# Kernel tuning notes

Hardware: AMD Instinct MI355X
Metric: run time of the kernel (lower is better)

The kernel has to match this reference:

```python
import jax, jax.numpy as jnp
import numpy as np

B, T, C = 4, 1024, 768
H, HS = 12, 64           # num_heads, head_size
VD = 2 * HS              # value dim per head


def setup_inputs() -> dict:
    key = jax.random.key(0)
    ks = jax.random.split(key, 16)
    s = 0.02
    inp = {
        "x": jax.random.normal(ks[0], (B, T, C), jnp.float32),
        "Wq1": jax.random.normal(ks[1], (H, C, HS), jnp.float32) * s,
        "Wk1": jax.random.normal(ks[2], (H, C, HS), jnp.float32) * s,
        "Wq2": jax.random.normal(ks[3], (H, C, HS), jnp.float32) * s,
        "Wk2": jax.random.normal(ks[4], (H, C, HS), jnp.float32) * s,
        "Wv": jax.random.normal(ks[5], (H, C, VD), jnp.float32) * s,
        "lq1": jax.random.normal(ks[6], (H, HS), jnp.float32) * 0.1,
        "lk1": jax.random.normal(ks[7], (H, HS), jnp.float32) * 0.1,
        "lq2": jax.random.normal(ks[8], (H, HS), jnp.float32) * 0.1,
        "lk2": jax.random.normal(ks[9], (H, HS), jnp.float32) * 0.1,
        "gn_w": jnp.ones((H * VD,), jnp.float32),
        "gn_b": jnp.zeros((H * VD,), jnp.float32),
        "Wp": jax.random.normal(ks[10], (C, H * VD), jnp.float32) * s,
        "bp": jnp.zeros((C,), jnp.float32),
        "layer_idx": 3,
    }
    return inp


def _diff_attn(x, Wq1, Wk1, Wq2, Wk2, Wv, lq1, lk1, lq2, lk2,
               gn_w, gn_b, Wp, bp, layer_idx):
    Bc, Tc, _ = x.shape
    scale = 1.0 / jnp.sqrt(jnp.float32(HS))
    # per-head projections: [B,H,T,HS]
    q1 = jnp.einsum('btc,hcd->bhtd', x, Wq1)
    k1 = jnp.einsum('btc,hcd->bhtd', x, Wk1)
    q2 = jnp.einsum('btc,hcd->bhtd', x, Wq2)
    k2 = jnp.einsum('btc,hcd->bhtd', x, Wk2)
    v = jnp.einsum('btc,hce->bhte', x, Wv)           # [B,H,T,2HS]
    mask = jnp.tril(jnp.ones((Tc, Tc), bool))         # causal
    neg = jnp.float32(-jnp.inf)
    a1 = jnp.einsum('bhtd,bhsd->bhts', q1, k1) * scale
    a2 = jnp.einsum('bhtd,bhsd->bhts', q2, k2) * scale
    a1 = jax.nn.softmax(jnp.where(mask, a1, neg), axis=-1)
    a2 = jax.nn.softmax(jnp.where(mask, a2, neg), axis=-1)
    # dynamic lambda init, per get_lambda
    li = jnp.float32(layer_idx)
    dyn = 0.8 - 0.6 * jnp.exp(-0.3 * (li - 1.0))
    lam = jnp.mean(jnp.exp(lq1 * lk1) - jnp.exp(lq2 * lk2) + dyn, axis=-1)  # [H]
    diff = a1 - lam[None, :, None, None] * a2
    out = jnp.einsum('bhts,bhse->bhte', diff, v)      # [B,H,T,2HS]
    out = out.transpose(0, 2, 1, 3).reshape(Bc, Tc, H * VD)
    # GroupLayerNorm == full layernorm over last dim (unbiased=False var)
    mu = out.mean(-1, keepdims=True)
    var = jnp.mean((out - mu) ** 2, axis=-1, keepdims=True)
    out = (out - mu) / jnp.sqrt(var + 1e-5) * gn_w + gn_b
    out = out * 0.2  # (1 - lambda_init_buffer=0.8), buffer never updated
    return out @ Wp.T + bp


def reference(x, Wq1, Wk1, Wq2, Wk2, Wv, lq1, lk1, lq2, lk2,
              gn_w, gn_b, Wp, bp, layer_idx):
    return _diff_attn(x, Wq1, Wk1, Wq2, Wk2, Wv, lq1, lk1, lq2, lk2,
                      gn_w, gn_b, Wp, bp, layer_idx)
```

## Files before the change

### kernel.cpp

```cpp
#include <hip/hip_runtime.h>
#include <hip/hip_bf16.h>

#define Bc   4
#define Tc   1024
#define Cc   768
#define Hc   12
#define HSc  64
#define VDc  128
#define NQKV 4608
#define YLD  3072
#define NROWS 4096
#define HVD  1536

#define Q1OFF 0
#define K1OFF 768
#define Q2OFF 1536
#define K2OFF 2304

typedef __bf16 bf16x8 __attribute__((ext_vector_type(8)));
typedef float f32x4 __attribute__((ext_vector_type(4)));
typedef unsigned int u32x4 __attribute__((ext_vector_type(4)));

#define EXP2SCALE 0.18033688011112042f

static __device__ __forceinline__ float bf2f(unsigned short s) {
    return __uint_as_float(((unsigned int)s) << 16);
}
static __device__ __forceinline__ unsigned short f2bf(float f) {
    unsigned int u = __float_as_uint(f);
    unsigned int r = (u + 0x7FFFu + ((u >> 16) & 1u)) >> 16;
    return (unsigned short)r;
}
static __device__ __forceinline__ unsigned int pack2bf(float lo, float hi) {
    unsigned int a = (__float_as_uint(lo) + 0x8000u) >> 16;
    unsigned int b = (__float_as_uint(hi) + 0x8000u) & 0xFFFF0000u;
    return a | b;
}
static __device__ __forceinline__ float fast_exp2(float x) {
    float r;
    asm("v_exp_f32 %0, %1" : "=v"(r) : "v"(x));
    return r;
}

static __device__ __forceinline__ void load16_lds(const void* g, void* l) {
    __builtin_amdgcn_global_load_lds(
        (const __attribute__((address_space(1))) void*)g,
        (__attribute__((address_space(3))) void*)l, 16, 0, 0);
}

__global__ __launch_bounds__(256) void prep(
    const float* __restrict__ x, const float* __restrict__ Wp,
    const float* __restrict__ lq1, const float* __restrict__ lk1,
    const float* __restrict__ lq2, const float* __restrict__ lk2,
    const int* __restrict__ layer_idx,
    const float* __restrict__ Wq1, const float* __restrict__ Wk1,
    const float* __restrict__ Wq2, const float* __restrict__ Wk2,
    const float* __restrict__ Wv,
    unsigned short* __restrict__ Xb, unsigned short* __restrict__ Wpb,
    float* __restrict__ lam, float* __restrict__ outz,
    unsigned short* __restrict__ WcatT)
{
    __shared__ float tile[64][65];
    int bid = blockIdx.x, tid = threadIdx.x;
    if (bid < 3072) {
        size_t i = (size_t)bid * 256 + tid;
        float4 v = *(const float4*)(x + i * 4);
        ushort4 u;
        u.x = f2bf(v.x); u.y = f2bf(v.y); u.z = f2bf(v.z); u.w = f2bf(v.w);
        *(ushort4*)(Xb + i * 4) = u;
    } else if (bid < 4224) {
        size_t i = (size_t)(bid - 3072) * 256 + tid;
        float4 v = *(const float4*)(Wp + i * 4);
        ushort4 u;
        u.x = f2bf(v.x); u.y = f2bf(v.y); u.z = f2bf(v.z); u.w = f2bf(v.w);
        *(ushort4*)(Wpb + i * 4) = u;
    } else if (bid < 4236) {
        if (tid < 64) {
            int h = bid - 4224, l = tid;
            float li = (float)layer_idx[0];
            float dyn = 0.8f - 0.6f * expf(-0.3f * (li - 1.0f));
            int i = h * HSc + l;
            float v = expf(lq1[i] * lk1[i]) - expf(lq2[i] * lk2[i]) + dyn;
            #pragma unroll
            for (int off = 32; off; off >>= 1) v += __shfl_xor(v, off);
            if (l == 0) lam[h] = v * (1.0f / 64.0f);
        }
    } else if (bid < 7308) {
        size_t i = (size_t)(bid - 4236) * 256 + tid;
        float4 z = {0.f, 0.f, 0.f, 0.f};
        *(float4*)(outz + i * 4) = z;
    } else {
        int t = bid - 7308;
        int kt = t % 12, nt = t / 12;
        int k0 = kt * 64, n0 = nt * 64;
        const float* src;
        int stride;
        if (n0 < 3072) {
            int which = n0 / 768, m = n0 - which * 768, h = m >> 6;
            const float* W = (which == 0) ? Wq1 : (which == 1) ? Wk1 : (which == 2) ? Wq2 : Wk2;
            src = W + ((size_t)h * 768 + k0) * 64;
            stride = 64;
        } else {
            int rel = n0 - 3072, h = rel >> 7, e0 = rel & 127;
            src = Wv + ((size_t)h * 768 + k0) * 128 + e0;
            stride = 128;
        }
        for (int i = tid; i < 4096; i += 256) {
            int kl = i >> 6, dl = i & 63;
            tile[dl][kl] = src[(size_t)kl * stride + dl];
        }
        __syncthreads();
        for (int i = tid; i < 4096; i += 256) {
            int nl = i >> 6, kl = i & 63;
            WcatT[(size_t)(n0 + nl) * 768 + k0 + kl] = f2bf(tile[nl][kl]);
        }
    }
}

template<int TN, int KD, int LDC, bool OUT_BIAS, bool SPLITV, int KSPLIT>
__global__ __launch_bounds__(256) void gemm_mfma(
    const unsigned short* __restrict__ A, const unsigned short* __restrict__ Bt,
    unsigned short* __restrict__ Cb, float* __restrict__ Cf,
    const float* __restrict__ bias, unsigned short* __restrict__ VtOut)
{
    constexpr int BN = TN * 32;
    constexpr int JB = TN / 2;
    constexpr int ASLOT = 128 * 64;
    constexpr int SLOT  = ASLOT + BN * 64;
    __shared__ unsigned short ring[2 * SLOT];
    int tid = threadIdx.x, lane = tid & 63, w = tid >> 6;
    int wm = w >> 1, wn = w & 1;

    int bid = blockIdx.x;
    int xcd = bid & 7;
    int idx = bid >> 3;
    int ks = 0;
    if (KSPLIT == 2) { ks = idx & 1; idx >>= 1; }
    int mi  = idx & 3;
    int ni  = idx >> 2;
    int m0 = (xcd * 4 + mi) * 128;
    int n0 = ni * BN;
    constexpr int KLOC = KD / KSPLIT;
    const int kBase = ks * KLOC;

    int lr = lane >> 2, lq = lane & 3;
    const unsigned short* gA[2];
    const unsigned short* gB[JB];
    #pragma unroll
    for (int j = 0; j < 2; ++j) {
        int row = w * 32 + j * 16 + lr;
        int qg = lq ^ ((row >> 1) & 3);
        gA[j] = A + (size_t)(m0 + row) * KD + kBase + qg * 8;
    }
    #pragma unroll
    for (int j = 0; j < JB; ++j) {
        int row = w * (JB * 16) + j * 16 + lr;
        int qg = lq ^ ((row >> 1) & 3);
        gB[j] = Bt + (size_t)(n0 + row) * KD + kBase + qg * 8;
    }

    int rr = lane & 15, qd = lane >> 4;
    int aOff[4], bOff[TN];
    #pragma unroll
    for (int i = 0; i < 4; ++i) {
        int row = wm * 64 + i * 16 + rr;
        int qs = qd ^ ((row >> 1) & 3);
        aOff[i] = row * 32 + qs * 8;
    }
    #pragma unroll
    for (int t = 0; t < TN; ++t) {
        int row = wn * (TN * 16) + t * 16 + rr;
        int qs = qd ^ ((row >> 1) & 3);
        bOff[t] = row * 32 + qs * 8;
    }

    auto stageG = [&](int k, int slot) {
        unsigned short* s = ring + slot * SLOT;
        int k64 = k * 64;
        load16_lds(gA[0] + k64,      s + (w * 2 + 0) * 512);
        load16_lds(gA[1] + k64,      s + (w * 2 + 1) * 512);
        load16_lds(gA[0] + k64 + 32, s + 4096 + (w * 2 + 0) * 512);
        load16_lds(gA[1] + k64 + 32, s + 4096 + (w * 2 + 1) * 512);
        #pragma unroll
        for (int j = 0; j < JB; ++j) {
            load16_lds(gB[j] + k64,      s + ASLOT + (w * JB + j) * 512);
            load16_lds(gB[j] + k64 + 32, s + ASLOT + BN * 32 + (w * JB + j) * 512);
        }
    };

    f32x4 acc[4][TN];
    #pragma unroll
    for (int i = 0; i < 4; ++i)
        #pragma unroll
        for (int t = 0; t < TN; ++t) acc[i][t] = {0.f, 0.f, 0.f, 0.f};

    constexpr int NT = KLOC / 64;
    stageG(0, 0);
    for (int k = 0; k < NT; ++k) {
        asm volatile("s_waitcnt vmcnt(0)\n\ts_barrier" ::: "memory");
        const unsigned short* s = ring + (k & 1) * SLOT;
        if (k + 1 < NT) stageG(k + 1, (k + 1) & 1);

        bf16x8 af0[4], af1[4], bf0[TN], bf1[TN];
        #pragma unroll
        for (int i = 0; i < 4; ++i) {
            af0[i] = *(const bf16x8*)(s + aOff[i]);
            af1[i] = *(const bf16x8*)(s + 4096 + aOff[i]);
        }
        #pragma unroll
        for (int t = 0; t < TN; ++t) {
            bf0[t] = *(const bf16x8*)(s + ASLOT + bOff[t]);
            bf1[t] = *(const bf16x8*)(s + ASLOT + BN * 32 + bOff[t]);
        }
        #pragma unroll
        for (int i = 0; i < 4; ++i)
            #pragma unroll
            for (int t = 0; t < TN; ++t) {
                acc[i][t] = __builtin_amdgcn_mfma_f32_16x16x32_bf16(af0[i], bf0[t], acc[i][t], 0, 0, 0);
                acc[i][t] = __builtin_amdgcn_mfma_f32_16x16x32_bf16(af1[i], bf1[t], acc[i][t], 0, 0, 0);
            }
    }

    #pragma unroll
    for (int t = 0; t < TN; ++t) {
        int col = n0 + wn * (TN * 16) + t * 16 + rr;
        if (SPLITV && col >= 3072) {
            int rel = col - 3072, hh = rel >> 7, e = rel & 127;
            #pragma unroll
            for (int i = 0; i < 4; ++i) {
                int row0 = m0 + wm * 64 + i * 16 + qd * 4;
                int b = row0 >> 10, tt = row0 & 1023;
                ushort4 pk;
                pk.x = f2bf(acc[i][t][0]); pk.y = f2bf(acc[i][t][1]);
                pk.z = f2bf(acc[i][t][2]); pk.w = f2bf(acc[i][t][3]);
                *(ushort4*)&VtOut[(size_t)((b * Hc + hh) * 128 + e) * 1024 + tt] = pk;
            }
        } else if (KSPLIT == 2) {
            float bv = (OUT_BIAS && ks == 0) ? bias[col] : 0.f;
            #pragma unroll
            for (int i = 0; i < 4; ++i) {
                #pragma unroll
                for (int r = 0; r < 4; ++r) {
                    int row = m0 + wm * 64 + i * 16 + qd * 4 + r;
                    atomicAdd(&Cf[(size_t)row * LDC + col], acc[i][t][r] + bv);
                }
            }
        } else {
            float bv = OUT_BIAS ? bias[col] : 0.f;
            #pragma unroll
            for (int i = 0; i < 4; ++i) {
                #pragma unroll
                for (int r = 0; r < 4; ++r) {
                    int row = m0 + wm * 64 + i * 16 + qd * 4 + r;
                    if (OUT_BIAS)
                        Cf[(size_t)row * LDC + col] = acc[i][t][r] + bv;
                    else
                        Cb[(size_t)row * LDC + col] = f2bf(acc[i][t][r]);
                }
            }
        }
    }
}

__global__ __launch_bounds__(256) void diff_attn_mfma(
    const unsigned short* __restrict__ Y, const unsigned short* __restrict__ Vt,
    const float* __restrict__ lam_buf, unsigned short* __restrict__ attn)
{
    __shared__ __align__(16) unsigned short KVring[2 * 16384];

    int bh = blockIdx.x;
    int b = bh / Hc, h = bh - b * Hc;
    int g = 15 - (int)blockIdx.y;
    int tid = threadIdx.x, lane = tid & 63, wv = tid >> 6;
    int cl = lane & 15, qd = lane >> 4;
    float lamv = lam_buf[h];
    size_t rowbase = (size_t)(b * Tc) * YLD;
    const int hq = h * HSc;
    const unsigned short* VtB = Vt + ((size_t)bh << 17);
    const f32x4 zero4 = {0.f, 0.f, 0.f, 0.f};

    int sub = wv & 1;
    int off8[8];
    int dstoff;
    if (wv < 2) {
        int ksrow = lane >> 3;
        int ksch  = (lane & 7) ^ ksrow;
        #pragma unroll
        for (int j = 0; j < 8; ++j) {
            int moff = (j < 4) ? K1OFF : K2OFF;
            off8[j] = ((j & 3) * 8 + ksrow) * YLD + moff + hq + ksch * 8;
        }
        dstoff = 0;
    } else {
        int vsel = lane >> 2;
        int vsch = (lane & 3) ^ ((vsel >> 1) & 3);
        #pragma unroll
        for (int s = 0; s < 8; ++s)
            off8[s] = (s * 16 + vsel) * 1024 + vsch * 8;
        dstoff = 8192;
    }

    auto stage = [&](int i, int slot) {
        int kt = 2 * i + sub;
        char* base = (char*)KVring + slot * 32768 + sub * 16384 + dstoff;
        const unsigned short* g0 = (wv < 2)
            ? (Y + rowbase + (size_t)(kt * 32) * YLD)
            : (VtB + kt * 32);
        #pragma unroll
        for (int j = 0; j < 8; ++j)
            load16_lds(g0 + off8[j], base + j * 1024);
    };

    int kfo[2][4], vfo[8];
    #pragma unroll
    for (int c = 0; c < 2; ++c) {
        int row = c * 16 + cl;
        #pragma unroll
        for (int j = 0; j < 4; ++j)
            kfo[c][j] = (j >> 1) * 4096 + row * 128 +
                        ((((j & 1) * 4 + qd) ^ (row & 7)) << 4);
    }
    #pragma unroll
    for (int ec = 0; ec < 8; ++ec) {
        int e = ec * 16 + cl;
        vfo[ec] = 8192 + e * 64 + ((qd ^ ((e >> 1) & 3)) << 4);
    }

    int idxA = ((32 * (qd & 1)) + cl) * 4;
    int idxB = idxA + 64;
    bool loHalf = (qd < 2);

    int qrow = g * 64 + wv * 16;

    stage(0, 0);

    size_t qoff = rowbase + (size_t)(qrow + cl) * YLD;
    bf16x8 q1a = *(const bf16x8*)(Y + qoff + Q1OFF + hq + qd * 8);
    bf16x8 q1b = *(const bf16x8*)(Y + qoff + Q1OFF + hq + 32 + qd * 8);
    bf16x8 q2a = *(const bf16x8*)(Y + qoff + Q2OFF + hq + qd * 8);
    bf16x8 q2b = *(const bf16x8*)(Y + qoff + Q2OFF + hq + 32 + qd * 8);

    f32x4 O1[8], O2[8];
    #pragma unroll
    for (int ec = 0; ec < 8; ++ec) { O1[ec] = zero4; O2[ec] = zero4; }
    float l1s = 0.f, l2s = 0.f;

    auto transform = [&](f32x4 S1[2], f32x4 S2[2], int kt,
                         bf16x8& pa1o, bf16x8& pa2o) {
        if (kt * 32 + 31 > qrow) {
            #pragma unroll
            for (int c = 0; c < 2; ++c) {
                int lim = qrow + cl - kt * 32 - c * 16 - qd * 4;
                #pragma unroll
                for (int r = 0; r < 4; ++r) {
                    if (r > lim) { S1[c][r] = -1e30f; S2[c][r] = -1e30f; }
                }
            }
        }
        float p1v[2][4], p2v[2][4];
        #pragma unroll
        for (int c = 0; c < 2; ++c) {
            #pragma unroll
            for (int r = 0; r < 4; ++r) {
                p1v[c][r] = fast_exp2(S1[c][r] * EXP2SCALE);
                p2v[c][r] = fast_exp2(S2[c][r] * EXP2SCALE);
                l1s += p1v[c][r];
                l2s += p2v[c][r];
            }
        }
        unsigned int s1m[2][2], s2m[2][2];
        #pragma unroll
        for (int c = 0; c < 2; ++c) {
            s1m[c][0] = pack2bf(p1v[c][0], p1v[c][1]);
            s1m[c][1] = pack2bf(p1v[c][2], p1v[c][3]);
            s2m[c][0] = pack2bf(p2v[c][0], p2v[c][1]);
            s2m[c][1] = pack2bf(p2v[c][2], p2v[c][3]);
        }
        u32x4 U1, U2;
        {
            int a00 = __builtin_amdgcn_ds_bpermute(idxA, (int)s1m[0][0]);
            int a10 = __builtin_amdgcn_ds_bpermute(idxA, (int)s1m[1][0]);
            int a01 = __builtin_amdgcn_ds_bpermute(idxA, (int)s1m[0][1]);
            int a11 = __builtin_amdgcn_ds_bpermute(idxA, (int)s1m[1][1]);
            int b00 = __builtin_amdgcn_ds_bpermute(idxB, (int)s1m[0][0]);
            int b10 = __builtin_amdgcn_ds_bpermute(idxB, (int)s1m[1][0]);
            int b01 = __builtin_amdgcn_ds_bpermute(idxB, (int)s1m[0][1]);
            int b11 = __builtin_amdgcn_ds_bpermute(idxB, (int)s1m[1][1]);
            U1[0] = (unsigned)(loHalf ? a00 : a10);
            U1[1] = (unsigned)(loHalf ? a01 : a11);
            U1[2] = (unsigned)(loHalf ? b00 : b10);
            U1[3] = (unsigned)(loHalf ? b01 : b11);
        }
        {
            int a00 = __builtin_amdgcn_ds_bpermute(idxA, (int)s2m[0][0]);
            int a10 = __builtin_amdgcn_ds_bpermute(idxA, (int)s2m[1][0]);
            int a01 = __builtin_amdgcn_ds_bpermute(idxA, (int)s2m[0][1]);
            int a11 = __builtin_amdgcn_ds_bpermute(idxA, (int)s2m[1][1]);
            int b00 = __builtin_amdgcn_ds_bpermute(idxB, (int)s2m[0][0]);
            int b10 = __builtin_amdgcn_ds_bpermute(idxB, (int)s2m[1][0]);
            int b01 = __builtin_amdgcn_ds_bpermute(idxB, (int)s2m[0][1]);
            int b11 = __builtin_amdgcn_ds_bpermute(idxB, (int)s2m[1][1]);
            U2[0] = (unsigned)(loHalf ? a00 : a10);
            U2[1] = (unsigned)(loHalf ? a01 : a11);
            U2[2] = (unsigned)(loHalf ? b00 : b10);
            U2[3] = (unsigned)(loHalf ? b01 : b11);
        }
        pa1o = __builtin_bit_cast(bf16x8, U1);
        pa2o = __builtin_bit_cast(bf16x8, U2);
    };

    int NI = g + 1;
    for (int i = 0; i < NI; ++i) {
        asm volatile("s_waitcnt vmcnt(0)\n\ts_barrier" ::: "memory");
        const char* kbA = (const char*)KVring + (i & 1) * 32768;
        const char* kbB = kbA + 16384;
        if (i + 1 < NI) stage(i + 1, (i + 1) & 1);

        bf16x8 kfA[2][4], kfB[2][4];
        #pragma unroll
        for (int c = 0; c < 2; ++c)
            #pragma unroll
            for (int j = 0; j < 4; ++j) {
                kfA[c][j] = *(const bf16x8*)(kbA + kfo[c][j]);
                kfB[c][j] = *(const bf16x8*)(kbB + kfo[c][j]);
            }
        bf16x8 vfA[8];
        #pragma unroll
        for (int ec = 0; ec < 8; ++ec)
            vfA[ec] = *(const bf16x8*)(kbA + vfo[ec]);

        f32x4 S1A[2], S2A[2], S1B[2], S2B[2];
        #pragma unroll
        for (int c = 0; c < 2; ++c) {
            S1A[c] = zero4; S2A[c] = zero4; S1B[c] = zero4; S2B[c] = zero4;
        }
        #pragma unroll
        for (int c = 0; c < 2; ++c) {
            S1A[c] = __builtin_amdgcn_mfma_f32_16x16x32_bf16(kfA[c][0], q1a, S1A[c], 0, 0, 0);
            S1A[c] = __builtin_amdgcn_mfma_f32_16x16x32_bf16(kfA[c][1], q1b, S1A[c], 0, 0, 0);
            S2A[c] = __builtin_amdgcn_mfma_f32_16x16x32_bf16(kfA[c][2], q2a, S2A[c], 0, 0, 0);
            S2A[c] = __builtin_amdgcn_mfma_f32_16x16x32_bf16(kfA[c][3], q2b, S2A[c], 0, 0, 0);
            S1B[c] = __builtin_amdgcn_mfma_f32_16x16x32_bf16(kfB[c][0], q1a, S1B[c], 0, 0, 0);
            S1B[c] = __builtin_amdgcn_mfma_f32_16x16x32_bf16(kfB[c][1], q1b, S1B[c], 0, 0, 0);
            S2B[c] = __builtin_amdgcn_mfma_f32_16x16x32_bf16(kfB[c][2], q2a, S2B[c], 0, 0, 0);
            S2B[c] = __builtin_amdgcn_mfma_f32_16x16x32_bf16(kfB[c][3], q2b, S2B[c], 0, 0, 0);
        }

        bf16x8 pa1A, pa2A, pa1B, pa2B;
        transform(S1A, S2A, 2 * i, pa1A, pa2A);
        bf16x8 vfB[8];
        #pragma unroll
        for (int ec = 0; ec < 8; ++ec)
            vfB[ec] = *(const bf16x8*)(kbB + vfo[ec]);
        transform(S1B, S2B, 2 * i + 1, pa1B, pa2B);

        #pragma unroll
        for (int ec = 0; ec < 8; ++ec) {
            O1[ec] = __builtin_amdgcn_mfma_f32_16x16x32_bf16(pa1A, vfA[ec], O1[ec], 0, 0, 0);
            O2[ec] = __builtin_amdgcn_mfma_f32_16x16x32_bf16(pa2A, vfA[ec], O2[ec], 0, 0, 0);
        }
        #pragma unroll
        for (int ec = 0; ec < 8; ++ec) {
            O1[ec] = __builtin_amdgcn_mfma_f32_16x16x32_bf16(pa1B, vfB[ec], O1[ec], 0, 0, 0);
            O2[ec] = __builtin_amdgcn_mfma_f32_16x16x32_bf16(pa2B, vfB[ec], O2[ec], 0, 0, 0);
        }
    }

    l1s += __shfl_xor(l1s, 16); l1s += __shfl_xor(l1s, 32);
    l2s += __shfl_xor(l2s, 16); l2s += __shfl_xor(l2s, 32);
    float w1[4], w2[4];
    #pragma unroll
    for (int r = 0; r < 4; ++r) {
        float d1 = __shfl(l1s, qd * 4 + r);
        float d2 = __shfl(l2s, qd * 4 + r);
        w1[r] = 1.0f / d1;
        w2[r] = lamv / d2;
    }
    #pragma unroll
    for (int ec = 0; ec < 8; ++ec) {
        #pragma unroll
        for (int r = 0; r < 4; ++r) {
            size_t row = (size_t)(b * Tc + qrow + qd * 4 + r);
            attn[row * HVD + h * VDc + ec * 16 + cl] =
                f2bf(O1[ec][r] * w1[r] - O2[ec][r] * w2[r]);
        }
    }
}

__global__ __launch_bounds__(128) void ln_inplace(
    unsigned short* __restrict__ attn,
    const float* __restrict__ gnw, const float* __restrict__ gnb)
{
    int row = blockIdx.x, tid = threadIdx.x;
    unsigned short* p = attn + (size_t)row * HVD;
    float v[12];
    float s = 0.f, sq = 0.f;
    #pragma unroll
    for (int j = 0; j < 3; ++j) {
        int g = tid + j * 128;
        ushort4 u = *(const ushort4*)(p + g * 4);
        float x0 = bf2f(u.x), x1 = bf2f(u.y), x2 = bf2f(u.z), x3 = bf2f(u.w);
        v[j * 4 + 0] = x0; v[j * 4 + 1] = x1; v[j * 4 + 2] = x2; v[j * 4 + 3] = x3;
        s += x0 + x1 + x2 + x3;
        sq = fmaf(x0, x0, sq); sq = fmaf(x1, x1, sq);
        sq = fmaf(x2, x2, sq); sq = fmaf(x3, x3, sq);
    }
    #pragma unroll
    for (int off = 32; off; off >>= 1) { s += __shfl_xor(s, off); sq += __shfl_xor(sq, off); }
    __shared__ float ss[2], sqs[2];
    if ((tid & 63) == 0) { ss[tid >> 6] = s; sqs[tid >> 6] = sq; }
    __syncthreads();
    float S = ss[0] + ss[1], Q = sqs[0] + sqs[1];
    float mu = S * (1.0f / HVD);
    float rstd = rsqrtf(Q * (1.0f / HVD) - mu * mu + 1e-5f);
    #pragma unroll
    for (int j = 0; j < 3; ++j) {
        int g = tid + j * 128;
        float4 gw = *(const float4*)(gnw + g * 4);
        float4 gb = *(const float4*)(gnb + g * 4);
        ushort4 o;
        o.x = f2bf(((v[j * 4 + 0] - mu) * rstd * gw.x + gb.x) * 0.2f);
        o.y = f2bf(((v[j * 4 + 1] - mu) * rstd * gw.y + gb.y) * 0.2f);
        o.z = f2bf(((v[j * 4 + 2] - mu) * rstd * gw.z + gb.z) * 0.2f);
        o.w = f2bf(((v[j * 4 + 3] - mu) * rstd * gw.w + gb.w) * 0.2f);
        *(ushort4*)(p + g * 4) = o;
    }
}

extern "C" void kernel_launch(void* const* d_in, const int* in_sizes, int n_in,
                              void* d_out, int out_size, void* d_ws, size_t ws_size,
                              hipStream_t stream)
{
    const float* x   = (const float*)d_in[0];
    const float* Wq1 = (const float*)d_in[1];
    const float* Wk1 = (const float*)d_in[2];
    const float* Wq2 = (const float*)d_in[3];
    const float* Wk2 = (const float*)d_in[4];
    const float* Wv  = (const float*)d_in[5];
    const float* lq1 = (const float*)d_in[6];
    const float* lk1 = (const float*)d_in[7];
    const float* lq2 = (const float*)d_in[8];
    const float* lk2 = (const float*)d_in[9];
    const float* gnw = (const float*)d_in[10];
    const float* gnb = (const float*)d_in[11];
    const float* Wp  = (const float*)d_in[12];
    const float* bp  = (const float*)d_in[13];
    const int*   lidx = (const int*)d_in[14];
    float* out = (float*)d_out;

    char* w = (char*)d_ws;
    unsigned short* WcatT = (unsigned short*)(w);
    unsigned short* Xb    = (unsigned short*)(w + 7077888);
    unsigned short* Y     = (unsigned short*)(w + 13369344);
    unsigned short* VtW   = (unsigned short*)(w + 38535168);
    unsigned short* attn  = (unsigned short*)(w + 51118080);
    unsigned short* Wpb   = (unsigned short*)(w + 63700992);
    float* lam            = (float*)(w + 66060288);

    prep<<<dim3(8172), 256, 0, stream>>>(x, Wp, lq1, lk1, lq2, lk2, lidx,
                                         Wq1, Wk1, Wq2, Wk2, Wv,
                                         Xb, Wpb, lam, out, WcatT);
    gemm_mfma<4, 768, YLD, false, true, 1><<<dim3(1152), 256, 0, stream>>>(
        Xb, WcatT, Y, nullptr, nullptr, VtW);
    diff_attn_mfma<<<dim3(Bc * Hc, 16), 256, 0, stream>>>(Y, VtW, lam, attn);
    ln_inplace<<<dim3(NROWS), 128, 0, stream>>>(attn, gnw, gnb);
    gemm_mfma<2, HVD, Cc, true, false, 2><<<dim3(768), 256, 0, stream>>>(
        attn, Wpb, nullptr, out, bp, nullptr);
}
```

Measured before the change: 235.6 us.

## Load V fragments directly from global memory instead of staging through LDS

Only the K1/K2 tiles are staged into the shared-memory ring now, with all four waves splitting the K staging. Each wave reads its V fragments straight from global memory into registers at the start of every iteration. This halves LDS usage, which may allow more resident blocks, and removes the LDS round trip for V. In exchange each wave fetches V redundantly through the cache hierarchy. Global-load latency may also become exposed before the PV MFMAs, since those loads are issued in the same iteration they are consumed.

```diff
diff --git a/kernel.cpp b/kernel.cpp
--- a/kernel.cpp
+++ b/kernel.cpp
@@ -266,7 +266,7 @@
     const unsigned short* __restrict__ Y, const unsigned short* __restrict__ Vt,
     const float* __restrict__ lam_buf, unsigned short* __restrict__ attn)
 {
-    __shared__ __align__(16) unsigned short KVring[2 * 16384];
+    __shared__ __align__(16) unsigned short Kring[2 * 8192];
 
     int bh = blockIdx.x;
     int b = bh / Hc, h = bh - b * Hc;
@@ -279,39 +279,28 @@
     const unsigned short* VtB = Vt + ((size_t)bh << 17);
     const f32x4 zero4 = {0.f, 0.f, 0.f, 0.f};
 
-    int sub = wv & 1;
-    int off8[8];
-    int dstoff;
-    if (wv < 2) {
-        int ksrow = lane >> 3;
-        int ksch  = (lane & 7) ^ ksrow;
-        #pragma unroll
-        for (int j = 0; j < 8; ++j) {
-            int moff = (j < 4) ? K1OFF : K2OFF;
-            off8[j] = ((j & 3) * 8 + ksrow) * YLD + moff + hq + ksch * 8;
-        }
-        dstoff = 0;
-    } else {
-        int vsel = lane >> 2;
-        int vsch = (lane & 3) ^ ((vsel >> 1) & 3);
-        #pragma unroll
-        for (int s = 0; s < 8; ++s)
-            off8[s] = (s * 16 + vsel) * 1024 + vsch * 8;
-        dstoff = 8192;
+    int sub   = wv & 1;
+    int halfK = wv >> 1;
+    int ksrow = lane >> 3;
+    int ksch  = (lane & 7) ^ ksrow;
+    int offk[4];
+    #pragma unroll
+    for (int j = 0; j < 4; ++j) {
+        int seg = halfK * 4 + j;
+        int moff = (seg < 4) ? K1OFF : K2OFF;
+        offk[j] = ((seg & 3) * 8 + ksrow) * YLD + moff + hq + ksch * 8;
     }
 
     auto stage = [&](int i, int slot) {
         int kt = 2 * i + sub;
-        char* base = (char*)KVring + slot * 32768 + sub * 16384 + dstoff;
-        const unsigned short* g0 = (wv < 2)
-            ? (Y + rowbase + (size_t)(kt * 32) * YLD)
-            : (VtB + kt * 32);
-        #pragma unroll
-        for (int j = 0; j < 8; ++j)
-            load16_lds(g0 + off8[j], base + j * 1024);
+        char* base = (char*)Kring + slot * 16384 + sub * 8192 + halfK * 4096;
+        const unsigned short* g0 = Y + rowbase + (size_t)(kt * 32) * YLD;
+        #pragma unroll
+        for (int j = 0; j < 4; ++j)
+            load16_lds(g0 + offk[j], base + j * 1024);
     };
 
-    int kfo[2][4], vfo[8];
+    int kfo[2][4];
     #pragma unroll
     for (int c = 0; c < 2; ++c) {
         int row = c * 16 + cl;
@@ -320,11 +309,10 @@
             kfo[c][j] = (j >> 1) * 4096 + row * 128 +
                         ((((j & 1) * 4 + qd) ^ (row & 7)) << 4);
     }
-    #pragma unroll
-    for (int ec = 0; ec < 8; ++ec) {
-        int e = ec * 16 + cl;
-        vfo[ec] = 8192 + e * 64 + ((qd ^ ((e >> 1) & 3)) << 4);
-    }
+    int vgo[8];
+    #pragma unroll
+    for (int ec = 0; ec < 8; ++ec)
+        vgo[ec] = ((ec * 16 + cl) << 10) + qd * 8;
 
     int idxA = ((32 * (qd & 1)) + cl) * 4;
     int idxB = idxA + 64;
@@ -412,8 +400,16 @@
     int NI = g + 1;
     for (int i = 0; i < NI; ++i) {
         asm volatile("s_waitcnt vmcnt(0)\n\ts_barrier" ::: "memory");
-        const char* kbA = (const char*)KVring + (i & 1) * 32768;
-        const char* kbB = kbA + 16384;
+        const char* kbA = (const char*)Kring + (i & 1) * 16384;
+        const char* kbB = kbA + 8192;
+
+        bf16x8 vfA[8], vfB[8];
+        #pragma unroll
+        for (int ec = 0; ec < 8; ++ec)
+            vfA[ec] = *(const bf16x8*)(VtB + vgo[ec] + (2 * i) * 32);
+        #pragma unroll
+        for (int ec = 0; ec < 8; ++ec)
+            vfB[ec] = *(const bf16x8*)(VtB + vgo[ec] + (2 * i + 1) * 32);
         if (i + 1 < NI) stage(i + 1, (i + 1) & 1);
 
         bf16x8 kfA[2][4], kfB[2][4];
@@ -424,10 +420,6 @@
                 kfA[c][j] = *(const bf16x8*)(kbA + kfo[c][j]);
                 kfB[c][j] = *(const bf16x8*)(kbB + kfo[c][j]);
             }
-        bf16x8 vfA[8];
-        #pragma unroll
-        for (int ec = 0; ec < 8; ++ec)
-            vfA[ec] = *(const bf16x8*)(kbA + vfo[ec]);
 
         f32x4 S1A[2], S2A[2], S1B[2], S2B[2];
         #pragma unroll
@@ -448,10 +440,6 @@
 
         bf16x8 pa1A, pa2A, pa1B, pa2B;
         transform(S1A, S2A, 2 * i, pa1A, pa2A);
-        bf16x8 vfB[8];
-        #pragma unroll
-        for (int ec = 0; ec < 8; ++ec)
-            vfB[ec] = *(const bf16x8*)(kbB + vfo[ec]);
         transform(S1B, S2B, 2 * i + 1, pa1B, pa2B);
 
         #pragma unroll
```

Result: slower. 279.7 us (+18.7%).

## Double query rows per wave in diff attention to reuse K/V tiles

Applied to the files above, without the earlier changes.

Each workgroup now covers 128 query rows instead of 64, and each wave handles two 16-row query groups that share the K/V fragments loaded from LDS. This halves the number of workgroups and the K/V traffic per query row, since every staged tile serves twice as many rows. The cost is many more accumulator registers per wave, which lowers occupancy, plus fewer blocks (384) to spread across the CUs. Waves whose rows end before the current tile skip the compute but still join the barriers, so causal load imbalance inside a block grows.

```diff
diff --git a/kernel.cpp b/kernel.cpp
--- a/kernel.cpp
+++ b/kernel.cpp
@@ -270,7 +270,7 @@
 
     int bh = blockIdx.x;
     int b = bh / Hc, h = bh - b * Hc;
-    int g = 15 - (int)blockIdx.y;
+    int g = 7 - (int)blockIdx.y;
     int tid = threadIdx.x, lane = tid & 63, wv = tid >> 6;
     int cl = lane & 15, qd = lane >> 4;
     float lamv = lam_buf[h];
@@ -330,27 +330,36 @@
     int idxB = idxA + 64;
     bool loHalf = (qd < 2);
 
-    int qrow = g * 64 + wv * 16;
+    int qr0 = g * 128 + wv * 32;
+    int qr1 = qr0 + 16;
 
     stage(0, 0);
 
-    size_t qoff = rowbase + (size_t)(qrow + cl) * YLD;
-    bf16x8 q1a = *(const bf16x8*)(Y + qoff + Q1OFF + hq + qd * 8);
-    bf16x8 q1b = *(const bf16x8*)(Y + qoff + Q1OFF + hq + 32 + qd * 8);
-    bf16x8 q2a = *(const bf16x8*)(Y + qoff + Q2OFF + hq + qd * 8);
-    bf16x8 q2b = *(const bf16x8*)(Y + qoff + Q2OFF + hq + 32 + qd * 8);
-
-    f32x4 O1[8], O2[8];
-    #pragma unroll
-    for (int ec = 0; ec < 8; ++ec) { O1[ec] = zero4; O2[ec] = zero4; }
-    float l1s = 0.f, l2s = 0.f;
-
-    auto transform = [&](f32x4 S1[2], f32x4 S2[2], int kt,
-                         bf16x8& pa1o, bf16x8& pa2o) {
-        if (kt * 32 + 31 > qrow) {
+    size_t qoff0 = rowbase + (size_t)(qr0 + cl) * YLD;
+    bf16x8 q1a0 = *(const bf16x8*)(Y + qoff0 + Q1OFF + hq + qd * 8);
+    bf16x8 q1b0 = *(const bf16x8*)(Y + qoff0 + Q1OFF + hq + 32 + qd * 8);
+    bf16x8 q2a0 = *(const bf16x8*)(Y + qoff0 + Q2OFF + hq + qd * 8);
+    bf16x8 q2b0 = *(const bf16x8*)(Y + qoff0 + Q2OFF + hq + 32 + qd * 8);
+    size_t qoff1 = rowbase + (size_t)(qr1 + cl) * YLD;
+    bf16x8 q1a1 = *(const bf16x8*)(Y + qoff1 + Q1OFF + hq + qd * 8);
+    bf16x8 q1b1 = *(const bf16x8*)(Y + qoff1 + Q1OFF + hq + 32 + qd * 8);
+    bf16x8 q2a1 = *(const bf16x8*)(Y + qoff1 + Q2OFF + hq + qd * 8);
+    bf16x8 q2b1 = *(const bf16x8*)(Y + qoff1 + Q2OFF + hq + 32 + qd * 8);
+
+    f32x4 O1g0[8], O2g0[8], O1g1[8], O2g1[8];
+    #pragma unroll
+    for (int ec = 0; ec < 8; ++ec) {
+        O1g0[ec] = zero4; O2g0[ec] = zero4;
+        O1g1[ec] = zero4; O2g1[ec] = zero4;
+    }
+    float l1s0 = 0.f, l2s0 = 0.f, l1s1 = 0.f, l2s1 = 0.f;
+
+    auto transform = [&](f32x4 S1[2], f32x4 S2[2], int kt, int qrowX,
+                         float& l1s, float& l2s, bf16x8& pa1o, bf16x8& pa2o) {
+        if (kt * 32 + 31 > qrowX) {
             #pragma unroll
             for (int c = 0; c < 2; ++c) {
-                int lim = qrow + cl - kt * 32 - c * 16 - qd * 4;
+                int lim = qrowX + cl - kt * 32 - c * 16 - qd * 4;
                 #pragma unroll
                 for (int r = 0; r < 4; ++r) {
                     if (r > lim) { S1[c][r] = -1e30f; S2[c][r] = -1e30f; }
@@ -409,80 +418,112 @@
         pa2o = __builtin_bit_cast(bf16x8, U2);
     };
 
-    int NI = g + 1;
+    int NI = 2 * g + 2;
     for (int i = 0; i < NI; ++i) {
         asm volatile("s_waitcnt vmcnt(0)\n\ts_barrier" ::: "memory");
         const char* kbA = (const char*)KVring + (i & 1) * 32768;
         const char* kbB = kbA + 16384;
         if (i + 1 < NI) stage(i + 1, (i + 1) & 1);
 
-        bf16x8 kfA[2][4], kfB[2][4];
-        #pragma unroll
-        for (int c = 0; c < 2; ++c)
-            #pragma unroll
-            for (int j = 0; j < 4; ++j) {
-                kfA[c][j] = *(const bf16x8*)(kbA + kfo[c][j]);
-                kfB[c][j] = *(const bf16x8*)(kbB + kfo[c][j]);
-            }
-        bf16x8 vfA[8];
-        #pragma unroll
-        for (int ec = 0; ec < 8; ++ec)
-            vfA[ec] = *(const bf16x8*)(kbA + vfo[ec]);
-
-        f32x4 S1A[2], S2A[2], S1B[2], S2B[2];
-        #pragma unroll
-        for (int c = 0; c < 2; ++c) {
-            S1A[c] = zero4; S2A[c] = zero4; S1B[c] = zero4; S2B[c] = zero4;
-        }
-        #pragma unroll
-        for (int c = 0; c < 2; ++c) {
-            S1A[c] = __builtin_amdgcn_mfma_f32_16x16x32_bf16(kfA[c][0], q1a, S1A[c], 0, 0, 0);
-            S1A[c] = __builtin_amdgcn_mfma_f32_16x16x32_bf16(kfA[c][1], q1b, S1A[c], 0, 0, 0);
-            S2A[c] = __builtin_amdgcn_mfma_f32_16x16x32_bf16(kfA[c][2], q2a, S2A[c], 0, 0, 0);
-            S2A[c] = __builtin_amdgcn_mfma_f32_16x16x32_bf16(kfA[c][3], q2b, S2A[c], 0, 0, 0);
-            S1B[c] = __builtin_amdgcn_mfma_f32_16x16x32_bf16(kfB[c][0], q1a, S1B[c], 0, 0, 0);
-            S1B[c] = __builtin_amdgcn_mfma_f32_16x16x32_bf16(kfB[c][1], q1b, S1B[c], 0, 0, 0);
-            S2B[c] = __builtin_amdgcn_mfma_f32_16x16x32_bf16(kfB[c][2], q2a, S2B[c], 0, 0, 0);
-            S2B[c] = __builtin_amdgcn_mfma_f32_16x16x32_bf16(kfB[c][3], q2b, S2B[c], 0, 0, 0);
-        }
-
-        bf16x8 pa1A, pa2A, pa1B, pa2B;
-        transform(S1A, S2A, 2 * i, pa1A, pa2A);
-        bf16x8 vfB[8];
-        #pragma unroll
-        for (int ec = 0; ec < 8; ++ec)
-            vfB[ec] = *(const bf16x8*)(kbB + vfo[ec]);
-        transform(S1B, S2B, 2 * i + 1, pa1B, pa2B);
-
-        #pragma unroll
-        for (int ec = 0; ec < 8; ++ec) {
-            O1[ec] = __builtin_amdgcn_mfma_f32_16x16x32_bf16(pa1A, vfA[ec], O1[ec], 0, 0, 0);
-            O2[ec] = __builtin_amdgcn_mfma_f32_16x16x32_bf16(pa2A, vfA[ec], O2[ec], 0, 0, 0);
-        }
-        #pragma unroll
-        for (int ec = 0; ec < 8; ++ec) {
-            O1[ec] = __builtin_amdgcn_mfma_f32_16x16x32_bf16(pa1B, vfB[ec], O1[ec], 0, 0, 0);
-            O2[ec] = __builtin_amdgcn_mfma_f32_16x16x32_bf16(pa2B, vfB[ec], O2[ec], 0, 0, 0);
-        }
-    }
-
-    l1s += __shfl_xor(l1s, 16); l1s += __shfl_xor(l1s, 32);
-    l2s += __shfl_xor(l2s, 16); l2s += __shfl_xor(l2s, 32);
-    float w1[4], w2[4];
+        if (i * 64 <= qr1 + 15) {
+            bf16x8 kfA[2][4], kfB[2][4];
+            #pragma unroll
+            for (int c = 0; c < 2; ++c)
+                #pragma unroll
+                for (int j = 0; j < 4; ++j) {
+                    kfA[c][j] = *(const bf16x8*)(kbA + kfo[c][j]);
+                    kfB[c][j] = *(const bf16x8*)(kbB + kfo[c][j]);
+                }
+            bf16x8 vfA[8];
+            #pragma unroll
+            for (int ec = 0; ec < 8; ++ec)
+                vfA[ec] = *(const bf16x8*)(kbA + vfo[ec]);
+
+            f32x4 S1A0[2], S2A0[2], S1B0[2], S2B0[2];
+            f32x4 S1A1[2], S2A1[2], S1B1[2], S2B1[2];
+            #pragma unroll
+            for (int c = 0; c < 2; ++c) {
+                S1A0[c] = zero4; S2A0[c] = zero4; S1B0[c] = zero4; S2B0[c] = zero4;
+                S1A1[c] = zero4; S2A1[c] = zero4; S1B1[c] = zero4; S2B1[c] = zero4;
+            }
+            #pragma unroll
+            for (int c = 0; c < 2; ++c) {
+                S1A0[c] = __builtin_amdgcn_mfma_f32_16x16x32_bf16(kfA[c][0], q1a0, S1A0[c], 0, 0, 0);
+                S1A0[c] = __builtin_amdgcn_mfma_f32_16x16x32_bf16(kfA[c][1], q1b0, S1A0[c], 0, 0, 0);
+                S2A0[c] = __builtin_amdgcn_mfma_f32_16x16x32_bf16(kfA[c][2], q2a0, S2A0[c], 0, 0, 0);
+                S2A0[c] = __builtin_amdgcn_mfma_f32_16x16x32_bf16(kfA[c][3], q2b0, S2A0[c], 0, 0, 0);
+                S1A1[c] = __builtin_amdgcn_mfma_f32_16x16x32_bf16(kfA[c][0], q1a1, S1A1[c], 0, 0, 0);
+                S1A1[c] = __builtin_amdgcn_mfma_f32_16x16x32_bf16(kfA[c][1], q1b1, S1A1[c], 0, 0, 0);
+                S2A1[c] = __builtin_amdgcn_mfma_f32_16x16x32_bf16(kfA[c][2], q2a1, S2A1[c], 0, 0, 0);
+                S2A1[c] = __builtin_amdgcn_mfma_f32_16x16x32_bf16(kfA[c][3], q2b1, S2A1[c], 0, 0, 0);
+                S1B0[c] = __builtin_amdgcn_mfma_f32_16x16x32_bf16(kfB[c][0], q1a0, S1B0[c], 0, 0, 0);
+                S1B0[c] = __builtin_amdgcn_mfma_f32_16x16x32_bf16(kfB[c][1], q1b0, S1B0[c], 0, 0, 0);
+                S2B0[c] = __builtin_amdgcn_mfma_f32_16x16x32_bf16(kfB[c][2], q2a0, S2B0[c], 0, 0, 0);
+                S2B0[c] = __builtin_amdgcn_mfma_f32_16x16x32_bf16(kfB[c][3], q2b0, S2B0[c], 0, 0, 0);
+                S1B1[c] = __builtin_amdgcn_mfma_f32_16x16x32_bf16(kfB[c][0], q1a1, S1B1[c], 0, 0, 0);
+                S1B1[c] = __builtin_amdgcn_mfma_f32_16x16x32_bf16(kfB[c][1], q1b1, S1B1[c], 0, 0, 0);
+                S2B1[c] = __builtin_amdgcn_mfma_f32_16x16x32_bf16(kfB[c][2], q2a1, S2B1[c], 0, 0, 0);
+                S2B1[c] = __builtin_amdgcn_mfma_f32_16x16x32_bf16(kfB[c][3], q2b1, S2B1[c], 0, 0, 0);
+            }
+
+            bf16x8 pa1A0, pa2A0, pa1A1, pa2A1, pa1B0, pa2B0, pa1B1, pa2B1;
+            transform(S1A0, S2A0, 2 * i, qr0, l1s0, l2s0, pa1A0, pa2A0);
+            transform(S1A1, S2A1, 2 * i, qr1, l1s1, l2s1, pa1A1, pa2A1);
+            bf16x8 vfB[8];
+            #pragma unroll
+            for (int ec = 0; ec < 8; ++ec)
+                vfB[ec] = *(const bf16x8*)(kbB + vfo[ec]);
+            #pragma unroll
+            for (int ec = 0; ec < 8; ++ec) {
+                O1g0[ec] = __builtin_amdgcn_mfma_f32_16x16x32_bf16(pa1A0, vfA[ec], O1g0[ec], 0, 0, 0);
+                O2g0[ec] = __builtin_amdgcn_mfma_f32_16x16x32_bf16(pa2A0, vfA[ec], O2g0[ec], 0, 0, 0);
+            }
+            #pragma unroll
+            for (int ec = 0; ec < 8; ++ec) {
+                O1g1[ec] = __builtin_amdgcn_mfma_f32_16x16x32_bf16(pa1A1, vfA[ec], O1g1[ec], 0, 0, 0);
+                O2g1[ec] = __builtin_amdgcn_mfma_f32_16x16x32_bf16(pa2A1, vfA[ec], O2g1[ec], 0, 0, 0);
+            }
+            transform(S1B0, S2B0, 2 * i + 1, qr0, l1s0, l2s0, pa1B0, pa2B0);
+            transform(S1B1, S2B1, 2 * i + 1, qr1, l1s1, l2s1, pa1B1, pa2B1);
+            #pragma unroll
+            for (int ec = 0; ec < 8; ++ec) {
+                O1g0[ec] = __builtin_amdgcn_mfma_f32_16x16x32_bf16(pa1B0, vfB[ec], O1g0[ec], 0, 0, 0);
+                O2g0[ec] = __builtin_amdgcn_mfma_f32_16x16x32_bf16(pa2B0, vfB[ec], O2g0[ec], 0, 0, 0);
+            }
+            #pragma unroll
+            for (int ec = 0; ec < 8; ++ec) {
+                O1g1[ec] = __builtin_amdgcn_mfma_f32_16x16x32_bf16(pa1B1, vfB[ec], O1g1[ec], 0, 0, 0);
+                O2g1[ec] = __builtin_amdgcn_mfma_f32_16x16x32_bf16(pa2B1, vfB[ec], O2g1[ec], 0, 0, 0);
+            }
+        }
+    }
+
+    l1s0 += __shfl_xor(l1s0, 16); l1s0 += __shfl_xor(l1s0, 32);
+    l2s0 += __shfl_xor(l2s0, 16); l2s0 += __shfl_xor(l2s0, 32);
+    l1s1 += __shfl_xor(l1s1, 16); l1s1 += __shfl_xor(l1s1, 32);
+    l2s1 += __shfl_xor(l2s1, 16); l2s1 += __shfl_xor(l2s1, 32);
+    float w10[4], w20[4], w11[4], w21[4];
     #pragma unroll
     for (int r = 0; r < 4; ++r) {
-        float d1 = __shfl(l1s, qd * 4 + r);
-        float d2 = __shfl(l2s, qd * 4 + r);
-        w1[r] = 1.0f / d1;
-        w2[r] = lamv / d2;
+        float d10 = __shfl(l1s0, qd * 4 + r);
+        float d20 = __shfl(l2s0, qd * 4 + r);
+        float d11 = __shfl(l1s1, qd * 4 + r);
+        float d21 = __shfl(l2s1, qd * 4 + r);
+        w10[r] = 1.0f / d10;
+        w20[r] = lamv / d20;
+        w11[r] = 1.0f / d11;
+        w21[r] = lamv / d21;
     }
     #pragma unroll
     for (int ec = 0; ec < 8; ++ec) {
         #pragma unroll
         for (int r = 0; r < 4; ++r) {
-            size_t row = (size_t)(b * Tc + qrow + qd * 4 + r);
-            attn[row * HVD + h * VDc + ec * 16 + cl] =
-                f2bf(O1[ec][r] * w1[r] - O2[ec][r] * w2[r]);
+            size_t row0 = (size_t)(b * Tc + qr0 + qd * 4 + r);
+            attn[row0 * HVD + h * VDc + ec * 16 + cl] =
+                f2bf(O1g0[ec][r] * w10[r] - O2g0[ec][r] * w20[r]);
+            size_t row1 = (size_t)(b * Tc + qr1 + qd * 4 + r);
+            attn[row1 * HVD + h * VDc + ec * 16 + cl] =
+                f2bf(O1g1[ec][r] * w11[r] - O2g1[ec][r] * w21[r]);
         }
     }
 }
@@ -562,7 +603,7 @@
                                          Xb, Wpb, lam, out, WcatT);
     gemm_mfma<4, 768, YLD, false, true, 1><<<dim3(1152), 256, 0, stream>>>(
         Xb, WcatT, Y, nullptr, nullptr, VtW);
-    diff_attn_mfma<<<dim3(Bc * Hc, 16), 256, 0, stream>>>(Y, VtW, lam, attn);
+    diff_attn_mfma<<<dim3(Bc * Hc, 8), 256, 0, stream>>>(Y, VtW, lam, attn);
     ln_inplace<<<dim3(NROWS), 128, 0, stream>>>(attn, gnw, gnb);
     gemm_mfma<2, HVD, Cc, true, false, 2><<<dim3(768), 256, 0, stream>>>(
         attn, Wpb, nullptr, out, bp, nullptr);
```

New measurement: 235.9 us. Within noise of the previous version (+0.1%).
